# Kernel optimization log

Hardware: AMD Instinct MI355X
Metric: run time of the kernel (lower is better)

The kernel has to match this reference:

```python
import jax, jax.numpy as jnp
import numpy as np

# Dims: batch, queries, graph nodes, text len, hidden, heads, layers, ffn
B, NQ, NN, T, D, H, LAYERS, FF = 16, 32, 128, 352, 768, 8, 6, 3072
L = NQ + NN + T          # 512 total sequence length
HD = D // H              # 96 head dim
NEG = -1e9               # additive mask value (HF uses dtype min; -1e9 is equivalent post-softmax)
LN_EPS = 1e-12           # BERT LayerNorm eps


def _ln(x, g, b):
    m = x.mean(-1, keepdims=True)
    v = ((x - m) ** 2).mean(-1, keepdims=True)
    return (x - m) * jax.lax.rsqrt(v + LN_EPS) * g + b


def setup_inputs() -> dict:
    key = jax.random.key(0)
    ks = iter(jax.random.split(key, 32))

    def nrm(shape, s=0.02):
        return jax.random.normal(next(ks), shape, jnp.float32) * s

    return {
        "graph_node_features": jax.random.normal(next(ks), (B, NN, D), jnp.float32),
        "text_embeds": jax.random.normal(next(ks), (B, T, D), jnp.float32),
        "text_atts": jnp.ones((B, T), jnp.int32),
        "graph_mask": jnp.ones((B, NN), jnp.int32),
        "query_tokens": nrm((1, NQ, D), 1.0),   # nn.Parameter(torch.randn(...))
        "gproj_w": nrm((D, D)), "gproj_b": jnp.zeros((D,)),
        "pos_emb": nrm((L, D)), "tok_emb": nrm((D,)),  # token_type row 0
        "emb_ln_g": jnp.ones((D,)), "emb_ln_b": jnp.zeros((D,)),
        "qkv_w": nrm((LAYERS, D, 3 * D)), "qkv_b": jnp.zeros((LAYERS, 3 * D)),
        "ao_w": nrm((LAYERS, D, D)), "ao_b": jnp.zeros((LAYERS, D)),
        "ln1_g": jnp.ones((LAYERS, D)), "ln1_b": jnp.zeros((LAYERS, D)),
        "ff1_w": nrm((LAYERS, D, FF)), "ff1_b": jnp.zeros((LAYERS, FF)),
        "ff2_w": nrm((LAYERS, FF, D)), "ff2_b": jnp.zeros((LAYERS, D)),
        "ln2_g": jnp.ones((LAYERS, D)), "ln2_b": jnp.zeros((LAYERS, D)),
    }


def _itg_bias(text_atts, graph_mask):
    # Build the custom ITG prefix-LM mask: bidirectional over [queries|graph],
    # causal over text, and queries/graph blocked from attending to text.
    keep = jnp.concatenate(
        [jnp.ones((B, NQ), jnp.int32), graph_mask, text_atts], axis=1)  # [B, L]
    ts = NQ + NN
    idx = jnp.arange(L)
    is_text = idx >= ts
    pair = (keep[:, :, None] * keep[:, None, :]).astype(bool)          # padding mask
    causal_ok = jnp.where(is_text[:, None] & is_text[None, :],
                          idx[:, None] >= idx[None, :], True)           # tril in text block
    block_ok = ~((~is_text)[:, None] & is_text[None, :])                # prefix cannot see text
    mask = pair & causal_ok & block_ok                                  # [B, L, L]
    return jnp.where(mask, 0.0, NEG)[:, None, :, :]                     # [B, 1, L, L]


def reference(graph_node_features, text_embeds, text_atts, graph_mask,
              query_tokens, gproj_w, gproj_b, pos_emb, tok_emb,
              emb_ln_g, emb_ln_b, qkv_w, qkv_b, ao_w, ao_b,
              ln1_g, ln1_b, ff1_w, ff1_b, ff2_w, ff2_b, ln2_g, ln2_b):
    gfeat = graph_node_features @ gproj_w + gproj_b
    qtok = jnp.broadcast_to(query_tokens, (B, NQ, D))
    x = jnp.concatenate([qtok, gfeat, text_embeds], axis=1)             # [B, L, D]
    bias = _itg_bias(text_atts, graph_mask)

    # BERT embeddings (inputs_embeds path): + position + token_type(0), LN (dropout off)
    x = _ln(x + pos_emb[None] + tok_emb, emb_ln_g, emb_ln_b)

    scale = 1.0 / np.sqrt(HD)
    for i in range(LAYERS):
        qkv = x @ qkv_w[i] + qkv_b[i]
        q, k, v = jnp.split(qkv, 3, axis=-1)
        q = q.reshape(B, L, H, HD)
        k = k.reshape(B, L, H, HD)
        v = v.reshape(B, L, H, HD)
        s = jnp.einsum('bqhd,bkhd->bhqk', q, k) * scale + bias
        p = jax.nn.softmax(s, axis=-1)
        ctx = jnp.einsum('bhqk,bkhd->bqhd', p, v).reshape(B, L, D)
        x = _ln(x + ctx @ ao_w[i] + ao_b[i], ln1_g[i], ln1_b[i])
        h = jax.nn.gelu(x @ ff1_w[i] + ff1_b[i], approximate=False)
        x = _ln(x + h @ ff2_w[i] + ff2_b[i], ln2_g[i], ln2_b[i])

    return x[:, NQ + NN:, :]   # text_feats [B, T, D]
```

## Files before the change

kernel.cpp:

```cpp
#include <hip/hip_runtime.h>
#include <math.h>

typedef __bf16 bf16;
typedef __bf16 bf16x8 __attribute__((ext_vector_type(8)));
typedef float f32x4 __attribute__((ext_vector_type(4)));

#define NQ   32
#define NN_  128
#define TT   352
#define DD   768
#define NH   8
#define HDIM 96
#define LSEQ 512
#define TSPLIT 160
#define FFD  3072
#define NLAYER 6
#define NBATCH 16

#define GLOAD(srcp, dstp)                                                     \
    __builtin_amdgcn_global_load_lds(                                         \
        (const __attribute__((address_space(1))) void*)(srcp),                \
        (__attribute__((address_space(3))) void*)(dstp), 16, 0, 0)

template <int ACT>
__global__ __launch_bounds__(256) void gemm_bt(
    const bf16* __restrict__ A, const bf16* __restrict__ Bt,
    bf16* __restrict__ C, const float* __restrict__ bias,
    int K, int lda, int ldb, int ldc, float alpha, int Nstore)
{
    __shared__ __attribute__((aligned(16))) bf16 As[3 * 4096];
    __shared__ __attribute__((aligned(16))) bf16 Bs[3 * 4096];

    const int n0 = blockIdx.x * 128, m0 = blockIdx.y * 128;
    const int t = threadIdx.x;
    const int w = t >> 6, l = t & 63;
    const int wm = w >> 1, wn = w & 1;
    const int lr = l & 15, quad = l >> 4;

    f32x4 acc[4][4] = {};

    const int f0 = w * 1024 + l * 8;
    const int ra0 = f0 >> 5, ca0 = f0 & 31;
    const int ra1 = (f0 + 512) >> 5, ca1 = (f0 + 512) & 31;
    const bf16* a0 = A  + (size_t)(m0 + ra0) * lda + ca0;
    const bf16* a1 = A  + (size_t)(m0 + ra1) * lda + ca1;
    const bf16* b0 = Bt + (size_t)(n0 + ra0) * ldb + ca0;
    const bf16* b1 = Bt + (size_t)(n0 + ra1) * ldb + ca1;

    const int nt = K >> 5;

    {
        bf16* pA = &As[w * 1024];
        bf16* pB = &Bs[w * 1024];
        GLOAD(a0, pA);        GLOAD(a1, pA + 512);
        GLOAD(b0, pB);        GLOAD(b1, pB + 512);
        pA += 4096;  pB += 4096;
        GLOAD(a0 + 32, pA);   GLOAD(a1 + 32, pA + 512);
        GLOAD(b0 + 32, pB);   GLOAD(b1 + 32, pB + 512);
    }

    int cb = 0;
    int wb = 2;
    for (int T = 0; T < nt; ++T) {
        if (T == nt - 1) {
            asm volatile("s_waitcnt vmcnt(0)" ::: "memory");
        } else {
            asm volatile("s_waitcnt vmcnt(4)" ::: "memory");
        }
        __builtin_amdgcn_s_barrier();
        __builtin_amdgcn_sched_barrier(0);

        if (T + 2 < nt) {
            const int k0 = (T + 2) << 5;
            bf16* pA = &As[wb * 4096 + w * 1024];
            bf16* pB = &Bs[wb * 4096 + w * 1024];
            GLOAD(a0 + k0, pA);   GLOAD(a1 + k0, pA + 512);
            GLOAD(b0 + k0, pB);   GLOAD(b1 + k0, pB + 512);
        }

        const int cur = cb << 12;
        bf16x8 af[4], bf_[4];
#pragma unroll
        for (int i = 0; i < 4; ++i)
            af[i] = *(const bf16x8*)&As[cur + (wm * 64 + i * 16 + lr) * 32 + quad * 8];
#pragma unroll
        for (int j = 0; j < 4; ++j)
            bf_[j] = *(const bf16x8*)&Bs[cur + (wn * 64 + j * 16 + lr) * 32 + quad * 8];
#pragma unroll
        for (int i = 0; i < 4; ++i)
#pragma unroll
            for (int j = 0; j < 4; ++j)
                acc[i][j] = __builtin_amdgcn_mfma_f32_16x16x32_bf16(af[i], bf_[j], acc[i][j], 0, 0, 0);

        cb = (cb == 2) ? 0 : cb + 1;
        wb = (wb == 2) ? 0 : wb + 1;
    }

#pragma unroll
    for (int i = 0; i < 4; ++i) {
        const int grow = m0 + wm * 64 + i * 16 + quad * 4;
#pragma unroll
        for (int j = 0; j < 4; ++j) {
            const int gcol = n0 + wn * 64 + j * 16 + lr;
            if (gcol >= Nstore) continue;
            float bv = bias ? bias[gcol] : 0.0f;
#pragma unroll
            for (int r = 0; r < 4; ++r) {
                float v = acc[i][j][r] * alpha + bv;
                if (ACT == 1) v = 0.5f * v * (1.0f + erff(v * 0.70710678118654752f));
                C[(size_t)(grow + r) * ldc + gcol] = (bf16)v;
            }
        }
    }
}

__global__ __launch_bounds__(256) void flash_attn(
    const bf16* __restrict__ qkv, bf16* __restrict__ ctx,
    const int* __restrict__ tatts, const int* __restrict__ gmask)
{
    __shared__ __attribute__((aligned(16))) bf16 Qs[64 * 104];
    __shared__ __attribute__((aligned(16))) bf16 Ks[64 * 104];
    __shared__ __attribute__((aligned(16))) bf16 Vs[96 * 72];
    __shared__ __attribute__((aligned(16))) bf16 Ps[64 * 72];
    __shared__ int keep[512];

    const int qt = blockIdx.x;
    const int bh = blockIdx.y;
    const int b = bh >> 3, h = bh & 7;
    const int q0 = qt * 64;
    const int t = threadIdx.x;
    const int w = t >> 6, l = t & 63;
    const int lr = l & 15, quad = l >> 4;
    const float scale = 0.10206207261596577f;

    const bf16* qbase = qkv + (size_t)b * 512 * 2304 + h * 96;
    const bf16* kbase = qbase + 768;
    const bf16* vbase = qbase + 1536;

    for (int j = t; j < 512; j += 256)
        keep[j] = (j < NQ) ? 1 : (j < TSPLIT ? gmask[b * NN_ + j - NQ]
                                             : tatts[b * TT + j - TSPLIT]);

#pragma unroll
    for (int c = 0; c < 3; ++c) {
        const int idx = t * 8 + c * 2048;
        const int r = idx / 96, d = idx % 96;
        *(bf16x8*)&Qs[r * 104 + d] =
            *(const bf16x8*)&qbase[(size_t)(q0 + r) * 2304 + d];
    }
    __syncthreads();

    int ki[4];
    int ig[4];
#pragma unroll
    for (int r = 0; r < 4; ++r) {
        ig[r] = q0 + w * 16 + quad * 4 + r;
        ki[r] = keep[ig[r]];
    }

    float m_run[4] = {-1e30f, -1e30f, -1e30f, -1e30f};
    float l_run[4] = {0.f, 0.f, 0.f, 0.f};
    f32x4 oc[6] = {};

    const int JMAX = (qt < 3) ? 128 : q0;
    for (int j0 = 0; j0 <= JMAX; j0 += 64) {
        __syncthreads();
#pragma unroll
        for (int c = 0; c < 3; ++c) {
            const int idx = t * 8 + c * 2048;
            const int r = idx / 96, d = idx % 96;
            *(bf16x8*)&Ks[r * 104 + d] =
                *(const bf16x8*)&kbase[(size_t)(j0 + r) * 2304 + d];
            bf16x8 vv = *(const bf16x8*)&vbase[(size_t)(j0 + r) * 2304 + d];
#pragma unroll
            for (int jj = 0; jj < 8; ++jj)
                Vs[(d + jj) * 72 + r] = vv[jj];
        }
        __syncthreads();

        bf16x8 aq[3];
#pragma unroll
        for (int ds = 0; ds < 3; ++ds)
            aq[ds] = *(const bf16x8*)&Qs[(w * 16 + lr) * 104 + ds * 32 + quad * 8];
        f32x4 sc[4];
#pragma unroll
        for (int cb = 0; cb < 4; ++cb) {
            f32x4 a = {};
#pragma unroll
            for (int ds = 0; ds < 3; ++ds) {
                bf16x8 bk = *(const bf16x8*)&Ks[(cb * 16 + lr) * 104 + ds * 32 + quad * 8];
                a = __builtin_amdgcn_mfma_f32_16x16x32_bf16(aq[ds], bk, a, 0, 0, 0);
            }
            sc[cb] = a;
        }

        float tm[4] = {-1e30f, -1e30f, -1e30f, -1e30f};
#pragma unroll
        for (int cb = 0; cb < 4; ++cb) {
            const int jg = j0 + cb * 16 + lr;
            const int kj = keep[jg];
#pragma unroll
            for (int r = 0; r < 4; ++r) {
                const int i = ig[r];
                bool ok = ki[r] && kj;
                if (i < TSPLIT && jg >= TSPLIT) ok = false;
                if (i >= TSPLIT && jg >= TSPLIT && i < jg) ok = false;
                float s = sc[cb][r] * scale + (ok ? 0.f : -1e9f);
                sc[cb][r] = s;
                tm[r] = fmaxf(tm[r], s);
            }
        }
#pragma unroll
        for (int off = 1; off < 16; off <<= 1)
#pragma unroll
            for (int r = 0; r < 4; ++r)
                tm[r] = fmaxf(tm[r], __shfl_xor(tm[r], off));

        float alpha_[4], ts[4] = {0.f, 0.f, 0.f, 0.f};
#pragma unroll
        for (int r = 0; r < 4; ++r) {
            const float mn = fmaxf(m_run[r], tm[r]);
            alpha_[r] = __expf(m_run[r] - mn);
            m_run[r] = mn;
            l_run[r] *= alpha_[r];
        }
#pragma unroll
        for (int db = 0; db < 6; ++db)
#pragma unroll
            for (int r = 0; r < 4; ++r)
                oc[db][r] *= alpha_[r];

#pragma unroll
        for (int cb = 0; cb < 4; ++cb)
#pragma unroll
            for (int r = 0; r < 4; ++r) {
                const float p = __expf(sc[cb][r] - m_run[r]);
                ts[r] += p;
                Ps[(w * 16 + quad * 4 + r) * 72 + cb * 16 + lr] = (bf16)p;
            }
#pragma unroll
        for (int off = 1; off < 16; off <<= 1)
#pragma unroll
            for (int r = 0; r < 4; ++r)
                ts[r] += __shfl_xor(ts[r], off);
#pragma unroll
        for (int r = 0; r < 4; ++r) l_run[r] += ts[r];

        __syncthreads();

#pragma unroll
        for (int l0 = 0; l0 < 64; l0 += 32) {
            bf16x8 ap = *(const bf16x8*)&Ps[(w * 16 + lr) * 72 + l0 + quad * 8];
#pragma unroll
            for (int db = 0; db < 6; ++db) {
                bf16x8 bv = *(const bf16x8*)&Vs[(db * 16 + lr) * 72 + l0 + quad * 8];
                oc[db] = __builtin_amdgcn_mfma_f32_16x16x32_bf16(ap, bv, oc[db], 0, 0, 0);
            }
        }
    }

#pragma unroll
    for (int r = 0; r < 4; ++r) {
        const float inv = 1.f / l_run[r];
        bf16* orow = ctx + ((size_t)b * 512 + ig[r]) * 768 + h * 96;
#pragma unroll
        for (int db = 0; db < 6; ++db)
            orow[db * 16 + lr] = (bf16)(oc[db][r] * inv);
    }
}

__global__ void transpose_w(const float* __restrict__ in, bf16* __restrict__ out,
                            int R, int C)
{
    __shared__ bf16 tile[32][33];
    const int c0 = blockIdx.x * 32, r0 = blockIdx.y * 32;
    const int tx = threadIdx.x & 31, ty = threadIdx.x >> 5;
    for (int i = ty; i < 32; i += 8)
        tile[i][tx] = (bf16)in[(size_t)(r0 + i) * C + c0 + tx];
    __syncthreads();
    for (int i = ty; i < 32; i += 8)
        out[(size_t)(c0 + i) * R + r0 + tx] = tile[tx][i];
}

__global__ void cvt_bf16(const float* __restrict__ in, bf16* __restrict__ out, int n)
{
    const int idx = blockIdx.x * 256 + threadIdx.x;
    if (idx < n) out[idx] = (bf16)in[idx];
}

__device__ __forceinline__ void block_reduce_2(float& a, float& b)
{
#pragma unroll
    for (int off = 32; off; off >>= 1) {
        a += __shfl_xor(a, off);
        b += __shfl_xor(b, off);
    }
    __shared__ float sa[4], sb[4];
    const int w = threadIdx.x >> 6;
    if ((threadIdx.x & 63) == 0) { sa[w] = a; sb[w] = b; }
    __syncthreads();
    a = sa[0] + sa[1] + sa[2] + sa[3];
    b = sb[0] + sb[1] + sb[2] + sb[3];
}

__global__ void embed_ln(const float* __restrict__ qtok, const bf16* __restrict__ gfeat,
                         const float* __restrict__ text, const float* __restrict__ pos,
                         const float* __restrict__ tok, const float* __restrict__ g,
                         const float* __restrict__ bb, bf16* __restrict__ x)
{
    const int row = blockIdx.x;
    const int l = row & 511, b = row >> 9;
    const int t = threadIdx.x;

    float vals[3], s = 0.f, sq = 0.f;
#pragma unroll
    for (int c = 0; c < 3; ++c) {
        const int d = t + c * 256;
        float base;
        if (l < NQ)           base = qtok[(size_t)l * DD + d];
        else if (l < TSPLIT)  base = (float)gfeat[((size_t)b * NN_ + (l - NQ)) * DD + d];
        else                  base = text[((size_t)b * TT + (l - TSPLIT)) * DD + d];
        float v = base + pos[(size_t)l * DD + d] + tok[d];
        vals[c] = v; s += v; sq += v * v;
    }
    block_reduce_2(s, sq);
    const float mean = s * (1.f / 768.f);
    const float var = sq * (1.f / 768.f) - mean * mean;
    const float rs = rsqrtf(var + 1e-12f);
    bf16* o = x + (size_t)row * DD;
#pragma unroll
    for (int c = 0; c < 3; ++c) {
        const int d = t + c * 256;
        o[d] = (bf16)((vals[c] - mean) * rs * g[d] + bb[d]);
    }
}

__global__ void ln_rows(const bf16* __restrict__ X, const bf16* __restrict__ Y,
                        bf16* __restrict__ Out, const float* __restrict__ g,
                        const float* __restrict__ bb)
{
    const int row = blockIdx.x;
    const int t = threadIdx.x;
    const bf16* xr = X + (size_t)row * DD;
    const bf16* yr = Y + (size_t)row * DD;
    float vals[3], s = 0.f, sq = 0.f;
#pragma unroll
    for (int c = 0; c < 3; ++c) {
        const int d = t + c * 256;
        float v = (float)xr[d] + (float)yr[d];
        vals[c] = v; s += v; sq += v * v;
    }
    block_reduce_2(s, sq);
    const float mean = s * (1.f / 768.f);
    const float var = sq * (1.f / 768.f) - mean * mean;
    const float rs = rsqrtf(var + 1e-12f);
    bf16* o = Out + (size_t)row * DD;
#pragma unroll
    for (int c = 0; c < 3; ++c) {
        const int d = t + c * 256;
        o[d] = (bf16)((vals[c] - mean) * rs * g[d] + bb[d]);
    }
}

__global__ void copy_out(const bf16* __restrict__ x, float* __restrict__ out)
{
    const size_t idx = (size_t)blockIdx.x * 256 + threadIdx.x;
    const int d = idx % DD;
    const size_t row = idx / DD;
    const int t = row % TT;
    const int b = row / TT;
    out[idx] = (float)x[((size_t)b * LSEQ + TSPLIT + t) * DD + d];
}

static void launch_gemm(const bf16* A, const bf16* Bt, bf16* C, const float* bias,
                        int M, int K, int lda, int ldb, int ldc,
                        float alpha, int Nstore, int act, hipStream_t stream)
{
    dim3 grid((Nstore + 127) / 128, M / 128, 1);
    if (act)
        gemm_bt<1><<<grid, 256, 0, stream>>>(A, Bt, C, bias, K, lda, ldb, ldc, alpha, Nstore);
    else
        gemm_bt<0><<<grid, 256, 0, stream>>>(A, Bt, C, bias, K, lda, ldb, ldc, alpha, Nstore);
}

extern "C" void kernel_launch(void* const* d_in, const int* in_sizes, int n_in,
                              void* d_out, int out_size, void* d_ws, size_t ws_size,
                              hipStream_t stream)
{
    const float* gnf     = (const float*)d_in[0];
    const float* text    = (const float*)d_in[1];
    const int*   tatts   = (const int*)d_in[2];
    const int*   gmask   = (const int*)d_in[3];
    const float* qtok    = (const float*)d_in[4];
    const float* gproj_w = (const float*)d_in[5];
    const float* gproj_b = (const float*)d_in[6];
    const float* pos     = (const float*)d_in[7];
    const float* tok     = (const float*)d_in[8];
    const float* eg      = (const float*)d_in[9];
    const float* eb      = (const float*)d_in[10];
    const float* qkv_w   = (const float*)d_in[11];
    const float* qkv_b   = (const float*)d_in[12];
    const float* ao_w    = (const float*)d_in[13];
    const float* ao_b    = (const float*)d_in[14];
    const float* ln1g    = (const float*)d_in[15];
    const float* ln1b    = (const float*)d_in[16];
    const float* ff1_w   = (const float*)d_in[17];
    const float* ff1_b   = (const float*)d_in[18];
    const float* ff2_w   = (const float*)d_in[19];
    const float* ff2_b   = (const float*)d_in[20];
    const float* ln2g    = (const float*)d_in[21];
    const float* ln2b    = (const float*)d_in[22];
    float* out = (float*)d_out;

    bf16* ws   = (bf16*)d_ws;
    bf16* wt1  = ws;
    bf16* wt2  = wt1 + 2359296;
    bf16* x    = wt2 + 2359296;
    bf16* ctx  = x   + 6291456;
    bf16* t1   = ctx + 6291456;
    bf16* u    = t1  + 6291456;
    bf16* qkvb = u;
    bf16* hbuf = u;
    bf16* gfeat = t1;
    bf16* gnfb  = u;

    dim3 blk(256);

    cvt_bf16<<<6144, blk, 0, stream>>>(gnf, gnfb, 1572864);
    transpose_w<<<dim3(24, 24), blk, 0, stream>>>(gproj_w, wt1, 768, 768);
    launch_gemm(gnfb, wt1, gfeat, gproj_b, 2048, 768, 768, 768, 768,
                1.f, 768, 0, stream);
    embed_ln<<<8192, blk, 0, stream>>>(qtok, gfeat, text, pos, tok, eg, eb, x);

    for (int i = 0; i < NLAYER; ++i) {
        transpose_w<<<dim3(72, 24), blk, 0, stream>>>(
            qkv_w + (size_t)i * 768 * 2304, wt1, 768, 2304);
        launch_gemm(x, wt1, qkvb, qkv_b + i * 2304,
                    8192, 768, 768, 768, 2304, 1.f, 2304, 0, stream);
        flash_attn<<<dim3(8, 128), blk, 0, stream>>>(qkvb, ctx, tatts, gmask);
        transpose_w<<<dim3(24, 24), blk, 0, stream>>>(
            ao_w + (size_t)i * 589824, wt1, 768, 768);
        launch_gemm(ctx, wt1, t1, ao_b + i * 768,
                    8192, 768, 768, 768, 768, 1.f, 768, 0, stream);
        ln_rows<<<8192, blk, 0, stream>>>(x, t1, x, ln1g + i * 768, ln1b + i * 768);

        transpose_w<<<dim3(96, 24), blk, 0, stream>>>(
            ff1_w + (size_t)i * 2359296, wt1, 768, 3072);
        transpose_w<<<dim3(24, 96), blk, 0, stream>>>(
            ff2_w + (size_t)i * 2359296, wt2, 3072, 768);
        launch_gemm(x, wt1, hbuf, ff1_b + i * 3072,
                    8192, 768, 768, 768, 3072, 1.f, 3072, 1, stream);
        launch_gemm(hbuf, wt2, t1, ff2_b + i * 768,
                    8192, 3072, 3072, 3072, 768, 1.f, 768, 0, stream);
        ln_rows<<<8192, blk, 0, stream>>>(x, t1, x, ln2g + i * 768, ln2b + i * 768);
    }

    copy_out<<<16896, blk, 0, stream>>>(x, out);

    (void)in_sizes; (void)n_in; (void)out_size; (void)ws_size;
}
```

Before: 2.180 ms.

## Add 256x128 GEMM tile, split-K for N=768 GEMMs, fuse partial sums into LN

Adds a 512-thread GEMM variant with a 256x128 tile for the wide QKV and FF1 projections, which raises A-tile reuse and halves the block count. The N=768 GEMMs (attention output and FF2) now use split-K of 2 over blockIdx.z. Each half writes a bf16 partial to its own buffer, and only z=0 adds the bias. The LayerNorm kernel now sums three inputs so it also reduces the two partials, which is meant to fix the low occupancy of the 384-block grids. In exchange there is extra partial-sum traffic, partials rounded to bf16, and higher LDS use per block in the big-tile kernel.

```diff
diff --git a/kernel.cpp b/kernel.cpp
--- a/kernel.cpp
+++ b/kernel.cpp
@@ -26,10 +26,15 @@
 __global__ __launch_bounds__(256) void gemm_bt(
     const bf16* __restrict__ A, const bf16* __restrict__ Bt,
     bf16* __restrict__ C, const float* __restrict__ bias,
-    int K, int lda, int ldb, int ldc, float alpha, int Nstore)
+    int K, int lda, int ldb, int ldc, float alpha, int Nstore, size_t zstride)
 {
     __shared__ __attribute__((aligned(16))) bf16 As[3 * 4096];
     __shared__ __attribute__((aligned(16))) bf16 Bs[3 * 4096];
+
+    const int z = blockIdx.z;
+    A  += (size_t)z * K;
+    Bt += (size_t)z * K;
+    C  += (size_t)z * zstride;
 
     const int n0 = blockIdx.x * 128, m0 = blockIdx.y * 128;
     const int t = threadIdx.x;
@@ -59,8 +64,7 @@
         GLOAD(b0 + 32, pB);   GLOAD(b1 + 32, pB + 512);
     }
 
-    int cb = 0;
-    int wb = 2;
+    int cb = 0, wb = 2;
     for (int T = 0; T < nt; ++T) {
         if (T == nt - 1) {
             asm volatile("s_waitcnt vmcnt(0)" ::: "memory");
@@ -91,6 +95,97 @@
 #pragma unroll
             for (int j = 0; j < 4; ++j)
                 acc[i][j] = __builtin_amdgcn_mfma_f32_16x16x32_bf16(af[i], bf_[j], acc[i][j], 0, 0, 0);
+
+        cb = (cb == 2) ? 0 : cb + 1;
+        wb = (wb == 2) ? 0 : wb + 1;
+    }
+
+    const bool dob = (z == 0);
+#pragma unroll
+    for (int i = 0; i < 4; ++i) {
+        const int grow = m0 + wm * 64 + i * 16 + quad * 4;
+#pragma unroll
+        for (int j = 0; j < 4; ++j) {
+            const int gcol = n0 + wn * 64 + j * 16 + lr;
+            if (gcol >= Nstore) continue;
+            float bv = (bias && dob) ? bias[gcol] : 0.0f;
+#pragma unroll
+            for (int r = 0; r < 4; ++r) {
+                float v = acc[i][j][r] * alpha + bv;
+                if (ACT == 1) v = 0.5f * v * (1.0f + erff(v * 0.70710678118654752f));
+                C[(size_t)(grow + r) * ldc + gcol] = (bf16)v;
+            }
+        }
+    }
+}
+
+template <int ACT>
+__global__ __launch_bounds__(512) void gemm_bt8(
+    const bf16* __restrict__ A, const bf16* __restrict__ Bt,
+    bf16* __restrict__ C, const float* __restrict__ bias,
+    int K, int lda, int ldb, int ldc, float alpha, int Nstore)
+{
+    __shared__ __attribute__((aligned(16))) bf16 As[3 * 8192];
+    __shared__ __attribute__((aligned(16))) bf16 Bs[3 * 4096];
+
+    const int n0 = blockIdx.x * 128, m0 = blockIdx.y * 256;
+    const int t = threadIdx.x;
+    const int w = t >> 6, l = t & 63;
+    const int wm = w >> 1, wn = w & 1;
+    const int lr = l & 15, quad = l >> 4;
+
+    f32x4 acc[4][4] = {};
+
+    const int f0 = w * 512 + l * 8;
+    const int ra0 = f0 >> 5,          ca0 = f0 & 31;
+    const int ra1 = ((f0 + 4096) >> 5), ca1 = f0 & 31;
+    const bf16* a0 = A  + (size_t)(m0 + ra0) * lda + ca0;
+    const bf16* a1 = A  + (size_t)(m0 + ra1) * lda + ca1;
+    const bf16* b0 = Bt + (size_t)(n0 + ra0) * ldb + ca0;
+
+    const int nt = K >> 5;
+
+    {
+        bf16* pA = &As[w * 512];
+        bf16* pB = &Bs[w * 512];
+        GLOAD(a0, pA);        GLOAD(a1, pA + 4096);   GLOAD(b0, pB);
+        pA += 8192;  pB += 4096;
+        GLOAD(a0 + 32, pA);   GLOAD(a1 + 32, pA + 4096);  GLOAD(b0 + 32, pB);
+    }
+
+    int cb = 0, wb = 2;
+    for (int T = 0; T < nt; ++T) {
+        if (T == nt - 1) {
+            asm volatile("s_waitcnt vmcnt(0)" ::: "memory");
+        } else {
+            asm volatile("s_waitcnt vmcnt(3)" ::: "memory");
+        }
+        __builtin_amdgcn_s_barrier();
+        __builtin_amdgcn_sched_barrier(0);
+
+        if (T + 2 < nt) {
+            const int k0 = (T + 2) << 5;
+            bf16* pA = &As[wb * 8192 + w * 512];
+            bf16* pB = &Bs[wb * 4096 + w * 512];
+            GLOAD(a0 + k0, pA);  GLOAD(a1 + k0, pA + 4096);  GLOAD(b0 + k0, pB);
+        }
+
+        const int curA = cb * 8192, curB = cb * 4096;
+        bf16x8 af[4], bf_[4];
+#pragma unroll
+        for (int i = 0; i < 4; ++i)
+            af[i] = *(const bf16x8*)&As[curA + (wm * 64 + i * 16 + lr) * 32 + quad * 8];
+#pragma unroll
+        for (int j = 0; j < 4; ++j)
+            bf_[j] = *(const bf16x8*)&Bs[curB + (wn * 64 + j * 16 + lr) * 32 + quad * 8];
+
+        __builtin_amdgcn_s_setprio(1);
+#pragma unroll
+        for (int i = 0; i < 4; ++i)
+#pragma unroll
+            for (int j = 0; j < 4; ++j)
+                acc[i][j] = __builtin_amdgcn_mfma_f32_16x16x32_bf16(af[i], bf_[j], acc[i][j], 0, 0, 0);
+        __builtin_amdgcn_s_setprio(0);
 
         cb = (cb == 2) ? 0 : cb + 1;
         wb = (wb == 2) ? 0 : wb + 1;
@@ -335,19 +430,20 @@
     }
 }
 
-__global__ void ln_rows(const bf16* __restrict__ X, const bf16* __restrict__ Y,
-                        bf16* __restrict__ Out, const float* __restrict__ g,
-                        const float* __restrict__ bb)
+__global__ void ln_rows3(const bf16* __restrict__ X, const bf16* __restrict__ Y,
+                         const bf16* __restrict__ Z, bf16* __restrict__ Out,
+                         const float* __restrict__ g, const float* __restrict__ bb)
 {
     const int row = blockIdx.x;
     const int t = threadIdx.x;
     const bf16* xr = X + (size_t)row * DD;
     const bf16* yr = Y + (size_t)row * DD;
+    const bf16* zr = Z + (size_t)row * DD;
     float vals[3], s = 0.f, sq = 0.f;
 #pragma unroll
     for (int c = 0; c < 3; ++c) {
         const int d = t + c * 256;
-        float v = (float)xr[d] + (float)yr[d];
+        float v = (float)xr[d] + (float)yr[d] + (float)zr[d];
         vals[c] = v; s += v; sq += v * v;
     }
     block_reduce_2(s, sq);
@@ -374,13 +470,25 @@
 
 static void launch_gemm(const bf16* A, const bf16* Bt, bf16* C, const float* bias,
                         int M, int K, int lda, int ldb, int ldc,
-                        float alpha, int Nstore, int act, hipStream_t stream)
-{
-    dim3 grid((Nstore + 127) / 128, M / 128, 1);
+                        float alpha, int Nstore, int act, int ksplit, size_t zstride,
+                        hipStream_t stream)
+{
+    dim3 grid((Nstore + 127) / 128, M / 128, ksplit);
     if (act)
-        gemm_bt<1><<<grid, 256, 0, stream>>>(A, Bt, C, bias, K, lda, ldb, ldc, alpha, Nstore);
+        gemm_bt<1><<<grid, 256, 0, stream>>>(A, Bt, C, bias, K / ksplit, lda, ldb, ldc, alpha, Nstore, zstride);
     else
-        gemm_bt<0><<<grid, 256, 0, stream>>>(A, Bt, C, bias, K, lda, ldb, ldc, alpha, Nstore);
+        gemm_bt<0><<<grid, 256, 0, stream>>>(A, Bt, C, bias, K / ksplit, lda, ldb, ldc, alpha, Nstore, zstride);
+}
+
+static void launch_gemm8(const bf16* A, const bf16* Bt, bf16* C, const float* bias,
+                         int M, int K, int lda, int ldb, int ldc,
+                         float alpha, int Nstore, int act, hipStream_t stream)
+{
+    dim3 grid((Nstore + 127) / 128, M / 256, 1);
+    if (act)
+        gemm_bt8<1><<<grid, 512, 0, stream>>>(A, Bt, C, bias, K, lda, ldb, ldc, alpha, Nstore);
+    else
+        gemm_bt8<0><<<grid, 512, 0, stream>>>(A, Bt, C, bias, K, lda, ldb, ldc, alpha, Nstore);
 }
 
 extern "C" void kernel_launch(void* const* d_in, const int* in_sizes, int n_in,
@@ -421,38 +529,40 @@
     bf16* u    = t1  + 6291456;
     bf16* qkvb = u;
     bf16* hbuf = u;
+    bf16* t2   = u   + 25165824;
     bf16* gfeat = t1;
     bf16* gnfb  = u;
+    const size_t ZST = (size_t)(t2 - t1);
 
     dim3 blk(256);
 
     cvt_bf16<<<6144, blk, 0, stream>>>(gnf, gnfb, 1572864);
     transpose_w<<<dim3(24, 24), blk, 0, stream>>>(gproj_w, wt1, 768, 768);
     launch_gemm(gnfb, wt1, gfeat, gproj_b, 2048, 768, 768, 768, 768,
-                1.f, 768, 0, stream);
+                1.f, 768, 0, 1, 0, stream);
     embed_ln<<<8192, blk, 0, stream>>>(qtok, gfeat, text, pos, tok, eg, eb, x);
 
     for (int i = 0; i < NLAYER; ++i) {
         transpose_w<<<dim3(72, 24), blk, 0, stream>>>(
             qkv_w + (size_t)i * 768 * 2304, wt1, 768, 2304);
-        launch_gemm(x, wt1, qkvb, qkv_b + i * 2304,
-                    8192, 768, 768, 768, 2304, 1.f, 2304, 0, stream);
+        launch_gemm8(x, wt1, qkvb, qkv_b + i * 2304,
+                     8192, 768, 768, 768, 2304, 1.f, 2304, 0, stream);
         flash_attn<<<dim3(8, 128), blk, 0, stream>>>(qkvb, ctx, tatts, gmask);
         transpose_w<<<dim3(24, 24), blk, 0, stream>>>(
             ao_w + (size_t)i * 589824, wt1, 768, 768);
         launch_gemm(ctx, wt1, t1, ao_b + i * 768,
-                    8192, 768, 768, 768, 768, 1.f, 768, 0, stream);
-        ln_rows<<<8192, blk, 0, stream>>>(x, t1, x, ln1g + i * 768, ln1b + i * 768);
+                    8192, 768, 768, 768, 768, 1.f, 768, 0, 2, ZST, stream);
+        ln_rows3<<<8192, blk, 0, stream>>>(x, t1, t2, x, ln1g + i * 768, ln1b + i * 768);
 
         transpose_w<<<dim3(96, 24), blk, 0, stream>>>(
             ff1_w + (size_t)i * 2359296, wt1, 768, 3072);
         transpose_w<<<dim3(24, 96), blk, 0, stream>>>(
             ff2_w + (size_t)i * 2359296, wt2, 3072, 768);
-        launch_gemm(x, wt1, hbuf, ff1_b + i * 3072,
-                    8192, 768, 768, 768, 3072, 1.f, 3072, 1, stream);
+        launch_gemm8(x, wt1, hbuf, ff1_b + i * 3072,
+                     8192, 768, 768, 768, 3072, 1.f, 3072, 1, stream);
         launch_gemm(hbuf, wt2, t1, ff2_b + i * 768,
-                    8192, 3072, 3072, 3072, 768, 1.f, 768, 0, stream);
-        ln_rows<<<8192, blk, 0, stream>>>(x, t1, x, ln2g + i * 768, ln2b + i * 768);
+                    8192, 3072, 3072, 3072, 768, 1.f, 768, 0, 2, ZST, stream);
+        ln_rows3<<<8192, blk, 0, stream>>>(x, t1, t2, x, ln2g + i * 768, ln2b + i * 768);
     }
 
     copy_out<<<16896, blk, 0, stream>>>(x, out);
```

Result: no change. 2.141 ms (-1.8%).
